# Optimization experiments

Measured on AMD Instinct MI355X. Metric: run time of the kernel, lower is better.

The kernel has to match this reference:

```python
import jax, jax.numpy as jnp
import numpy as np

N_OFFSETS = [(1, 0), (1, 1), (0, 1), (-1, 1), (-1, 0), (-1, -1), (0, -1), (1, -1)]
DILATION = 1


def setup_inputs() -> dict:
    key = jax.random.key(0)
    feats = jax.random.normal(key, (8, 128, 256, 256), dtype=jnp.float32)
    return {"feats": feats}


def reference(feats):
    # feats: [B, C, H, W]
    d = DILATION
    B, C, H, W = feats.shape
    # channel-wise L2 normalize (no eps, matching torch .norm division)
    normed = feats / jnp.linalg.norm(feats, axis=1, keepdims=True)
    # reflect pad last two spatial dims by d
    padded = jnp.pad(normed, ((0, 0), (0, 0), (d, d), (d, d)), mode="reflect")
    # 8 shifted multiply + channel-sum correlations (fixed small offset set)
    corrs = jnp.concatenate(
        [
            jnp.sum(
                normed
                * padded[:, :, d - dx * d // d if False else d - dx:H + d - dx, d - dy:W + d - dy],
                axis=1,
                keepdims=True,
            )
            for dx, dy in [(ox * d, oy * d) for ox, oy in N_OFFSETS]
        ],
        axis=1,
    )  # [B, 8, H, W]
    return corrs
```

## Files before the change

### kernel.cpp

```cpp
#include <hip/hip_runtime.h>


#define BB 8
#define CC 128
#define HH 256
#define WW 256

__global__ __launch_bounds__(512) void featcorr_kernel(
    const float* __restrict__ feats, float* __restrict__ out) {
  const int w = blockIdx.x * 64 + threadIdx.x;
  const int h = blockIdx.y * 8 + threadIdx.y;
  const int b = blockIdx.z;

  const int hm = (h == 0) ? 1 : h - 1;
  const int hp = (h == HH - 1) ? HH - 2 : h + 1;
  const int wm = (w == 0) ? 1 : w - 1;
  const int wp = (w == WW - 1) ? WW - 2 : w + 1;

  const size_t HW = (size_t)HH * WW;
  const float* base = feats + (size_t)b * CC * HW;

  const int rm = hm * WW, r0 = h * WW, rp = hp * WW;
  const int o00 = rm + wm, o01 = rm + w, o02 = rm + wp;
  const int o10 = r0 + wm, o11 = r0 + w, o12 = r0 + wp;
  const int o20 = rp + wm, o21 = rp + w, o22 = rp + wp;

  float s00 = 0.f, s01 = 0.f, s02 = 0.f;
  float s10 = 0.f, s11 = 0.f, s12 = 0.f;
  float s20 = 0.f, s21 = 0.f, s22 = 0.f;
  float d0 = 0.f, d1 = 0.f, d2 = 0.f, d3 = 0.f;
  float d4 = 0.f, d5 = 0.f, d6 = 0.f, d7 = 0.f;

#pragma unroll 4
  for (int c = 0; c < CC; ++c) {
    const float* p = base + (size_t)c * HW;
    const float v00 = p[o00], v01 = p[o01], v02 = p[o02];
    const float v10 = p[o10], v11 = p[o11], v12 = p[o12];
    const float v20 = p[o20], v21 = p[o21], v22 = p[o22];
    s00 += v00 * v00; s01 += v01 * v01; s02 += v02 * v02;
    s10 += v10 * v10; s11 += v11 * v11; s12 += v12 * v12;
    s20 += v20 * v20; s21 += v21 * v21; s22 += v22 * v22;
    d0 += v11 * v01;
    d1 += v11 * v00;
    d2 += v11 * v10;
    d3 += v11 * v20;
    d4 += v11 * v21;
    d5 += v11 * v22;
    d6 += v11 * v12;
    d7 += v11 * v02;
  }

  const float i00 = rsqrtf(s00), i01 = rsqrtf(s01), i02 = rsqrtf(s02);
  const float i10 = rsqrtf(s10), i11 = rsqrtf(s11), i12 = rsqrtf(s12);
  const float i20 = rsqrtf(s20), i21 = rsqrtf(s21), i22 = rsqrtf(s22);

  float* o = out + (size_t)b * 8 * HW + (size_t)h * WW + w;
  o[0 * HW] = d0 * i11 * i01;
  o[1 * HW] = d1 * i11 * i00;
  o[2 * HW] = d2 * i11 * i10;
  o[3 * HW] = d3 * i11 * i20;
  o[4 * HW] = d4 * i11 * i21;
  o[5 * HW] = d5 * i11 * i22;
  o[6 * HW] = d6 * i11 * i12;
  o[7 * HW] = d7 * i11 * i02;
}

extern "C" void kernel_launch(void* const* d_in, const int* in_sizes, int n_in,
                              void* d_out, int out_size, void* d_ws, size_t ws_size,
                              hipStream_t stream) {
  const float* feats = (const float*)d_in[0];
  float* out = (float*)d_out;
  dim3 block(64, 8, 1);
  dim3 grid(WW / 64, HH / 8, BB);
  featcorr_kernel<<<grid, block, 0, stream>>>(feats, out);
}
```

Measured before the change: 427.5 us.

## Vectorize rows with float4 and lane shuffles, split channels across waves

Each block now handles one full image row. Each lane loads four adjacent pixels per row as float4 and gets the left and right neighbours through wavefront shuffles, so it no longer issues nine scalar loads per channel. The 128 channels are split across four waves, and their partial sums are combined with a tree reduction in LDS before one wave writes float4 outputs. This is meant to cut the number of load instructions and redundant neighbour fetches. In exchange it needs 44 accumulators per thread, uses LDS with several barriers, and leaves three of the four waves idle during the output phase.

```diff
diff --git a/kernel.cpp b/kernel.cpp
--- a/kernel.cpp
+++ b/kernel.cpp
@@ -5,64 +5,147 @@
 #define CC 128
 #define HH 256
 #define WW 256
+#define CSPLIT 4
+#define CPW (CC / CSPLIT)
 
-__global__ __launch_bounds__(512) void featcorr_kernel(
+#define SQT(j) acc[(j)]
+#define SQM(j) acc[4 + (j)]
+#define SQB(j) acc[8 + (j)]
+#define DD(k, j) acc[12 + (k)*4 + (j)]
+
+__global__ __launch_bounds__(256) void featcorr_kernel(
     const float* __restrict__ feats, float* __restrict__ out) {
-  const int w = blockIdx.x * 64 + threadIdx.x;
-  const int h = blockIdx.y * 8 + threadIdx.y;
-  const int b = blockIdx.z;
+  const int lane = threadIdx.x;
+  const int wy = threadIdx.y;
+  const int h = blockIdx.x;
+  const int b = blockIdx.y;
 
   const int hm = (h == 0) ? 1 : h - 1;
   const int hp = (h == HH - 1) ? HH - 2 : h + 1;
-  const int wm = (w == 0) ? 1 : w - 1;
-  const int wp = (w == WW - 1) ? WW - 2 : w + 1;
 
   const size_t HW = (size_t)HH * WW;
-  const float* base = feats + (size_t)b * CC * HW;
+  const int col0 = lane * 4;
 
-  const int rm = hm * WW, r0 = h * WW, rp = hp * WW;
-  const int o00 = rm + wm, o01 = rm + w, o02 = rm + wp;
-  const int o10 = r0 + wm, o11 = r0 + w, o12 = r0 + wp;
-  const int o20 = rp + wm, o21 = rp + w, o22 = rp + wp;
+  const float* pT = feats + ((size_t)b * CC + wy * CPW) * HW + (size_t)hm * WW + col0;
+  const float* pM = feats + ((size_t)b * CC + wy * CPW) * HW + (size_t)h * WW + col0;
+  const float* pB = feats + ((size_t)b * CC + wy * CPW) * HW + (size_t)hp * WW + col0;
 
-  float s00 = 0.f, s01 = 0.f, s02 = 0.f;
-  float s10 = 0.f, s11 = 0.f, s12 = 0.f;
-  float s20 = 0.f, s21 = 0.f, s22 = 0.f;
-  float d0 = 0.f, d1 = 0.f, d2 = 0.f, d3 = 0.f;
-  float d4 = 0.f, d5 = 0.f, d6 = 0.f, d7 = 0.f;
+  float acc[44];
+#pragma unroll
+  for (int a = 0; a < 44; ++a) acc[a] = 0.f;
 
-#pragma unroll 4
-  for (int c = 0; c < CC; ++c) {
-    const float* p = base + (size_t)c * HW;
-    const float v00 = p[o00], v01 = p[o01], v02 = p[o02];
-    const float v10 = p[o10], v11 = p[o11], v12 = p[o12];
-    const float v20 = p[o20], v21 = p[o21], v22 = p[o22];
-    s00 += v00 * v00; s01 += v01 * v01; s02 += v02 * v02;
-    s10 += v10 * v10; s11 += v11 * v11; s12 += v12 * v12;
-    s20 += v20 * v20; s21 += v21 * v21; s22 += v22 * v22;
-    d0 += v11 * v01;
-    d1 += v11 * v00;
-    d2 += v11 * v10;
-    d3 += v11 * v20;
-    d4 += v11 * v21;
-    d5 += v11 * v22;
-    d6 += v11 * v12;
-    d7 += v11 * v02;
+#pragma unroll 2
+  for (int c = 0; c < CPW; ++c) {
+    const float4 t4 = *(const float4*)pT;
+    const float4 m4 = *(const float4*)pM;
+    const float4 b4 = *(const float4*)pB;
+    pT += HW; pM += HW; pB += HW;
+
+    float T[6], M[6], B[6];
+    T[1] = t4.x; T[2] = t4.y; T[3] = t4.z; T[4] = t4.w;
+    M[1] = m4.x; M[2] = m4.y; M[3] = m4.z; M[4] = m4.w;
+    B[1] = b4.x; B[2] = b4.y; B[3] = b4.z; B[4] = b4.w;
+
+    const float tL = __shfl_up(t4.w, 1), mL = __shfl_up(m4.w, 1), bL = __shfl_up(b4.w, 1);
+    const float tR = __shfl_down(t4.x, 1), mR = __shfl_down(m4.x, 1), bR = __shfl_down(b4.x, 1);
+    T[0] = (lane == 0) ? t4.y : tL;
+    M[0] = (lane == 0) ? m4.y : mL;
+    B[0] = (lane == 0) ? b4.y : bL;
+    T[5] = (lane == 63) ? t4.z : tR;
+    M[5] = (lane == 63) ? m4.z : mR;
+    B[5] = (lane == 63) ? b4.z : bR;
+
+#pragma unroll
+    for (int j = 0; j < 4; ++j) {
+      SQT(j) += T[j + 1] * T[j + 1];
+      SQM(j) += M[j + 1] * M[j + 1];
+      SQB(j) += B[j + 1] * B[j + 1];
+      const float mc = M[j + 1];
+      DD(0, j) += mc * T[j + 1];
+      DD(1, j) += mc * T[j];
+      DD(2, j) += mc * M[j];
+      DD(3, j) += mc * B[j];
+      DD(4, j) += mc * B[j + 1];
+      DD(5, j) += mc * B[j + 2];
+      DD(6, j) += mc * M[j + 2];
+      DD(7, j) += mc * T[j + 2];
+    }
   }
 
-  const float i00 = rsqrtf(s00), i01 = rsqrtf(s01), i02 = rsqrtf(s02);
-  const float i10 = rsqrtf(s10), i11 = rsqrtf(s11), i12 = rsqrtf(s12);
-  const float i20 = rsqrtf(s20), i21 = rsqrtf(s21), i22 = rsqrtf(s22);
+  __shared__ float lds[2][44][64];
+  if (wy == 1) {
+#pragma unroll
+    for (int a = 0; a < 44; ++a) lds[0][a][lane] = acc[a];
+  }
+  if (wy == 3) {
+#pragma unroll
+    for (int a = 0; a < 44; ++a) lds[1][a][lane] = acc[a];
+  }
+  __syncthreads();
+  if (wy == 0) {
+#pragma unroll
+    for (int a = 0; a < 44; ++a) acc[a] += lds[0][a][lane];
+  }
+  if (wy == 2) {
+#pragma unroll
+    for (int a = 0; a < 44; ++a) acc[a] += lds[1][a][lane];
+  }
+  __syncthreads();
+  if (wy == 2) {
+#pragma unroll
+    for (int a = 0; a < 44; ++a) lds[0][a][lane] = acc[a];
+  }
+  __syncthreads();
 
-  float* o = out + (size_t)b * 8 * HW + (size_t)h * WW + w;
-  o[0 * HW] = d0 * i11 * i01;
-  o[1 * HW] = d1 * i11 * i00;
-  o[2 * HW] = d2 * i11 * i10;
-  o[3 * HW] = d3 * i11 * i20;
-  o[4 * HW] = d4 * i11 * i21;
-  o[5 * HW] = d5 * i11 * i22;
-  o[6 * HW] = d6 * i11 * i12;
-  o[7 * HW] = d7 * i11 * i02;
+  if (wy == 0) {
+#pragma unroll
+    for (int a = 0; a < 44; ++a) acc[a] += lds[0][a][lane];
+
+    float iT[4], iM[4], iB[4];
+#pragma unroll
+    for (int j = 0; j < 4; ++j) {
+      iT[j] = rsqrtf(SQT(j));
+      iM[j] = rsqrtf(SQM(j));
+      iB[j] = rsqrtf(SQB(j));
+    }
+    float IT[6], IM[6], IB[6];
+    IT[1] = iT[0]; IT[2] = iT[1]; IT[3] = iT[2]; IT[4] = iT[3];
+    IM[1] = iM[0]; IM[2] = iM[1]; IM[3] = iM[2]; IM[4] = iM[3];
+    IB[1] = iB[0]; IB[2] = iB[1]; IB[3] = iB[2]; IB[4] = iB[3];
+    const float itL = __shfl_up(iT[3], 1), imL = __shfl_up(iM[3], 1), ibL = __shfl_up(iB[3], 1);
+    const float itR = __shfl_down(iT[0], 1), imR = __shfl_down(iM[0], 1), ibR = __shfl_down(iB[0], 1);
+    IT[0] = (lane == 0) ? iT[1] : itL;
+    IM[0] = (lane == 0) ? iM[1] : imL;
+    IB[0] = (lane == 0) ? iB[1] : ibL;
+    IT[5] = (lane == 63) ? iT[2] : itR;
+    IM[5] = (lane == 63) ? iM[2] : imR;
+    IB[5] = (lane == 63) ? iB[2] : ibR;
+
+    float* obase = out + ((size_t)b * 8) * HW + (size_t)h * WW + col0;
+#pragma unroll
+    for (int k = 0; k < 8; ++k) {
+      float4 o;
+      float v[4];
+#pragma unroll
+      for (int j = 0; j < 4; ++j) {
+        const float ic = iM[j];
+        float in;
+        switch (k) {
+          case 0: in = IT[j + 1]; break;
+          case 1: in = IT[j];     break;
+          case 2: in = IM[j];     break;
+          case 3: in = IB[j];     break;
+          case 4: in = IB[j + 1]; break;
+          case 5: in = IB[j + 2]; break;
+          case 6: in = IM[j + 2]; break;
+          default: in = IT[j + 2]; break;
+        }
+        v[j] = DD(k, j) * ic * in;
+      }
+      o.x = v[0]; o.y = v[1]; o.z = v[2]; o.w = v[3];
+      *(float4*)(obase + (size_t)k * HW) = o;
+    }
+  }
 }
 
 extern "C" void kernel_launch(void* const* d_in, const int* in_sizes, int n_in,
@@ -70,7 +153,7 @@
                               hipStream_t stream) {
   const float* feats = (const float*)d_in[0];
   float* out = (float*)d_out;
-  dim3 block(64, 8, 1);
-  dim3 grid(WW / 64, HH / 8, BB);
+  dim3 block(64, CSPLIT, 1);
+  dim3 grid(HH, BB, 1);
   featcorr_kernel<<<grid, block, 0, stream>>>(feats, out);
 }
```

Result: faster. 384.9 us (-9.9%).

## Tile two rows by full width per wave with float4 loads and split-channel reduction

Applied to the files above, without the earlier changes.

Each block now handles two full output rows. Every lane loads a float4 of four columns from four input rows per channel, and horizontal neighbours come from wave shuffles rather than redundant scattered loads. The channel loop is split across two waves whose 80 accumulators are combined through shared memory, and rows are remapped so neighbouring blocks are spread out. This is meant to cut the redundant 9-point global loads and the per-thread load count, at the cost of heavy register pressure from 80 accumulators and fewer threads per block.

```diff
diff --git a/kernel.cpp b/kernel.cpp
--- a/kernel.cpp
+++ b/kernel.cpp
@@ -5,64 +5,144 @@
 #define CC 128
 #define HH 256
 #define WW 256
+#define CPH (CC / 2)
 
-__global__ __launch_bounds__(512) void featcorr_kernel(
+#define DOTS(BASE, up, mid, dn, rU, rM_, rD)                                 \
+  {                                                                          \
+    acc[BASE+0]  += mid.x*up.x;  acc[BASE+1]  += mid.y*up.y;         \
+    acc[BASE+2]  += mid.z*up.z;  acc[BASE+3]  += mid.w*up.w;                 \
+    acc[BASE+5]  += mid.y*up.x;  acc[BASE+6]  += mid.z*up.y;         \
+    acc[BASE+7]  += mid.w*up.z;  acc[BASE+4]  += rM_*up.w;                   \
+    acc[BASE+9]  += mid.y*mid.x; acc[BASE+10] += mid.z*mid.y;        \
+    acc[BASE+11] += mid.w*mid.z;        \
+    acc[BASE+13] += mid.y*dn.x;  acc[BASE+14] += mid.z*dn.y;         \
+    acc[BASE+15] += mid.w*dn.z;  acc[BASE+12] += rM_*dn.w;                   \
+    acc[BASE+16] += mid.x*dn.x;  acc[BASE+17] += mid.y*dn.y;         \
+    acc[BASE+18] += mid.z*dn.z;  acc[BASE+19] += mid.w*dn.w;                 \
+    acc[BASE+20] += mid.x*dn.y;  acc[BASE+21] += mid.y*dn.z;         \
+    acc[BASE+22] += mid.z*dn.w;  acc[BASE+23] += mid.w*rD;                   \
+    acc[BASE+24] += mid.x*mid.y; acc[BASE+25] += mid.y*mid.z;        \
+    acc[BASE+26] += mid.z*mid.w; acc[BASE+27] += mid.w*rM_;                  \
+    acc[BASE+28] += mid.x*up.y;  acc[BASE+29] += mid.y*up.z;         \
+    acc[BASE+30] += mid.z*up.w;  acc[BASE+31] += mid.w*rU;                   \
+  }
+
+#define FIXB(Dbase)                                                          \
+  {                                                                          \
+    const float g1 = __shfl_up(acc[Dbase+4],  1);                            \
+    const float g2 = __shfl_up(acc[Dbase+27], 1);    \
+    const float g3 = __shfl_up(acc[Dbase+12], 1);                            \
+    acc[Dbase+4]  = (lane == 0) ? acc[Dbase+28] : g1;                        \
+    acc[Dbase+8]  = (lane == 0) ? acc[Dbase+24] : g2;                        \
+    acc[Dbase+12] = (lane == 0) ? acc[Dbase+20] : g3;                        \
+    if (lane == 63) {                                                        \
+      acc[Dbase+23] = acc[Dbase+15];                                         \
+      acc[Dbase+27] = acc[Dbase+11];                                         \
+      acc[Dbase+31] = acc[Dbase+7];                                          \
+    }                                                                        \
+  }
+
+#define EXT(e, ip)                                                           \
+  {                                                                          \
+    e[1] = ip[0]; e[2] = ip[1]; e[3] = ip[2]; e[4] = ip[3];                  \
+    const float l = __shfl_up(ip[3], 1);                                     \
+    const float r = __shfl_down(ip[0], 1);                                   \
+    e[0] = (lane == 0) ? ip[1] : l;                                          \
+    e[5] = (lane == 63) ? ip[2] : r;                                         \
+  }
+
+#define EMIT_K(k, arr, off)                                                  \
+  {                                                                          \
+    float4 o;                                                                \
+    o.x = acc[Dbase+(k)*4+0] * eC[1] * arr[0+off];                           \
+    o.y = acc[Dbase+(k)*4+1] * eC[2] * arr[1+off];                           \
+    o.z = acc[Dbase+(k)*4+2] * eC[3] * arr[2+off];                           \
+    o.w = acc[Dbase+(k)*4+3] * eC[4] * arr[3+off];                           \
+    *(float4*)(obase + (size_t)(k)*HW) = o;                                  \
+  }
+
+__global__ __launch_bounds__(128) void featcorr_kernel(
     const float* __restrict__ feats, float* __restrict__ out) {
-  const int w = blockIdx.x * 64 + threadIdx.x;
-  const int h = blockIdx.y * 8 + threadIdx.y;
-  const int b = blockIdx.z;
+  const int lane = threadIdx.x;
+  const int cs = threadIdx.y;
+  const int bx = blockIdx.x;
+  const int h0 = (((bx & 7) << 4) | (bx >> 3)) * 2;
+  const int b = blockIdx.y;
 
-  const int hm = (h == 0) ? 1 : h - 1;
-  const int hp = (h == HH - 1) ? HH - 2 : h + 1;
-  const int wm = (w == 0) ? 1 : w - 1;
-  const int wp = (w == WW - 1) ? WW - 2 : w + 1;
+  const int gT = (h0 == 0) ? 1 : h0 - 1;
+  const int gB = (h0 + 2 >= HH) ? HH - 2 : h0 + 2;
 
   const size_t HW = (size_t)HH * WW;
-  const float* base = feats + (size_t)b * CC * HW;
+  const int col0 = lane * 4;
 
-  const int rm = hm * WW, r0 = h * WW, rp = hp * WW;
-  const int o00 = rm + wm, o01 = rm + w, o02 = rm + wp;
-  const int o10 = r0 + wm, o11 = r0 + w, o12 = r0 + wp;
-  const int o20 = rp + wm, o21 = rp + w, o22 = rp + wp;
+  const float* base = feats + ((size_t)b * CC + (size_t)cs * CPH) * HW + col0;
+  const float* pT = base + (size_t)gT * WW;
+  const float* pM = base + (size_t)h0 * WW;
+  const float* pN = base + (size_t)(h0 + 1) * WW;
+  const float* pB = base + (size_t)gB * WW;
 
-  float s00 = 0.f, s01 = 0.f, s02 = 0.f;
-  float s10 = 0.f, s11 = 0.f, s12 = 0.f;
-  float s20 = 0.f, s21 = 0.f, s22 = 0.f;
-  float d0 = 0.f, d1 = 0.f, d2 = 0.f, d3 = 0.f;
-  float d4 = 0.f, d5 = 0.f, d6 = 0.f, d7 = 0.f;
+  float acc[80];
+#pragma unroll
+  for (int a = 0; a < 80; ++a) acc[a] = 0.f;
 
 #pragma unroll 4
-  for (int c = 0; c < CC; ++c) {
-    const float* p = base + (size_t)c * HW;
-    const float v00 = p[o00], v01 = p[o01], v02 = p[o02];
-    const float v10 = p[o10], v11 = p[o11], v12 = p[o12];
-    const float v20 = p[o20], v21 = p[o21], v22 = p[o22];
-    s00 += v00 * v00; s01 += v01 * v01; s02 += v02 * v02;
-    s10 += v10 * v10; s11 += v11 * v11; s12 += v12 * v12;
-    s20 += v20 * v20; s21 += v21 * v21; s22 += v22 * v22;
-    d0 += v11 * v01;
-    d1 += v11 * v00;
-    d2 += v11 * v10;
-    d3 += v11 * v20;
-    d4 += v11 * v21;
-    d5 += v11 * v22;
-    d6 += v11 * v12;
-    d7 += v11 * v02;
+  for (int c = 0; c < CPH; ++c) {
+    const float4 t  = *(const float4*)pT; pT += HW;
+    const float4 m  = *(const float4*)pM; pM += HW;
+    const float4 n  = *(const float4*)pN; pN += HW;
+    const float4 bt = *(const float4*)pB; pB += HW;
+    const float rT = __shfl_down(t.x, 1);
+    const float rM = __shfl_down(m.x, 1);
+    const float rN = __shfl_down(n.x, 1);
+    const float rB = __shfl_down(bt.x, 1);
+    acc[0]  += t.x*t.x;   acc[1]  += t.y*t.y;   acc[2]  += t.z*t.z;   acc[3]  += t.w*t.w;
+    acc[4]  += m.x*m.x;   acc[5]  += m.y*m.y;   acc[6]  += m.z*m.z;   acc[7]  += m.w*m.w;
+    acc[8]  += n.x*n.x;   acc[9]  += n.y*n.y;   acc[10] += n.z*n.z;   acc[11] += n.w*n.w;
+    acc[12] += bt.x*bt.x; acc[13] += bt.y*bt.y; acc[14] += bt.z*bt.z; acc[15] += bt.w*bt.w;
+    DOTS(16, t, m, n, rT, rM, rN);
+    DOTS(48, m, n, bt, rM, rN, rB);
   }
 
-  const float i00 = rsqrtf(s00), i01 = rsqrtf(s01), i02 = rsqrtf(s02);
-  const float i10 = rsqrtf(s10), i11 = rsqrtf(s11), i12 = rsqrtf(s12);
-  const float i20 = rsqrtf(s20), i21 = rsqrtf(s21), i22 = rsqrtf(s22);
+  __shared__ float red[80][64];
+  if (cs == 1) {
+#pragma unroll
+    for (int a = 0; a < 80; ++a) red[a][lane] = acc[a];
+  }
+  __syncthreads();
 
-  float* o = out + (size_t)b * 8 * HW + (size_t)h * WW + w;
-  o[0 * HW] = d0 * i11 * i01;
-  o[1 * HW] = d1 * i11 * i00;
-  o[2 * HW] = d2 * i11 * i10;
-  o[3 * HW] = d3 * i11 * i20;
-  o[4 * HW] = d4 * i11 * i21;
-  o[5 * HW] = d5 * i11 * i22;
-  o[6 * HW] = d6 * i11 * i12;
-  o[7 * HW] = d7 * i11 * i02;
+  if (cs == 0) {
+#pragma unroll
+    for (int a = 0; a < 80; ++a) acc[a] += red[a][lane];
+
+    FIXB(16);
+    FIXB(48);
+
+    float iT[4], iM[4], iN[4], iB[4];
+#pragma unroll
+    for (int j = 0; j < 4; ++j) {
+      iT[j] = rsqrtf(acc[j]);
+      iM[j] = rsqrtf(acc[4 + j]);
+      iN[j] = rsqrtf(acc[8 + j]);
+      iB[j] = rsqrtf(acc[12 + j]);
+    }
+    float eT[6], eM[6], eN[6], eB[6];
+    EXT(eT, iT); EXT(eM, iM); EXT(eN, iN); EXT(eB, iB);
+
+    {
+      const int Dbase = 16;
+      const float* eC = eM;
+      float* obase = out + ((size_t)b * 8) * HW + (size_t)h0 * WW + col0;
+      EMIT_K(0, eT, 1) EMIT_K(1, eT, 0) EMIT_K(2, eM, 0) EMIT_K(3, eN, 0)
+      EMIT_K(4, eN, 1) EMIT_K(5, eN, 2) EMIT_K(6, eM, 2) EMIT_K(7, eT, 2)
+    }
+    {
+      const int Dbase = 48;
+      const float* eC = eN;
+      float* obase = out + ((size_t)b * 8) * HW + (size_t)(h0 + 1) * WW + col0;
+      EMIT_K(0, eM, 1) EMIT_K(1, eM, 0) EMIT_K(2, eN, 0) EMIT_K(3, eB, 0)
+      EMIT_K(4, eB, 1) EMIT_K(5, eB, 2) EMIT_K(6, eN, 2) EMIT_K(7, eM, 2)
+    }
+  }
 }
 
 extern "C" void kernel_launch(void* const* d_in, const int* in_sizes, int n_in,
@@ -70,7 +150,7 @@
                               hipStream_t stream) {
   const float* feats = (const float*)d_in[0];
   float* out = (float*)d_out;
-  dim3 block(64, 8, 1);
-  dim3 grid(WW / 64, HH / 8, BB);
+  dim3 block(64, 2, 1);
+  dim3 grid(HH / 2, BB, 1);
   featcorr_kernel<<<grid, block, 0, stream>>>(feats, out);
 }
```

Result: faster. 364.8 us (-14.7%).
